# Performance work log

Measured on AMD Instinct MI355X. Metric: run time of the kernel, lower is better.

Reference implementation:

```python
import jax, jax.numpy as jnp
import numpy as np
from jax import lax

DS = 4  # downsample_factor

def setup_inputs() -> dict:
    key = jax.random.key(0)
    ks = jax.random.split(key, 7)
    B, C, H, W = 4, 256, 256, 256
    Cq = C // 16  # reduction=16
    return {
        "x":  jax.random.normal(ks[0], (B, C, H, W), dtype=jnp.float32),
        "Wq": jax.random.normal(ks[1], (Cq, C), dtype=jnp.float32) * 0.05,
        "bq": jax.random.normal(ks[2], (Cq,), dtype=jnp.float32) * 0.05,
        "Wk": jax.random.normal(ks[3], (Cq, C), dtype=jnp.float32) * 0.05,
        "bk": jax.random.normal(ks[4], (Cq,), dtype=jnp.float32) * 0.05,
        "Wv": jax.random.normal(ks[5], (C, C), dtype=jnp.float32) * 0.05,
        "bv": jax.random.normal(ks[6], (C,), dtype=jnp.float32) * 0.05,
    }

def reference(x, Wq, bq, Wk, bk, Wv, bv):
    B, C, H, W = x.shape
    # MaxPool2d(kernel=DS, stride=DS)
    xd = lax.reduce_window(x, -jnp.inf, lax.max,
                           (1, 1, DS, DS), (1, 1, DS, DS), 'VALID')
    h, w = xd.shape[2], xd.shape[3]
    N = h * w
    # 1x1 convs == channel-wise linear maps
    q = jnp.einsum('oc,bchw->bohw', Wq, xd) + bq[None, :, None, None]
    k = jnp.einsum('oc,bchw->bohw', Wk, xd) + bk[None, :, None, None]
    v = jnp.einsum('oc,bchw->bohw', Wv, xd) + bv[None, :, None, None]
    query = q.reshape(B, -1, N).transpose(0, 2, 1)   # [B, N, Cq]
    key_  = k.reshape(B, -1, N)                      # [B, Cq, N]
    value = v.reshape(B, C, N).transpose(0, 2, 1)    # [B, N, C]
    att = jnp.einsum('bnc,bcm->bnm', query, key_)    # [B, N, N]
    # global-mean threshold masking (zeros, not -inf, per original)
    att = jnp.where(att < att.mean(), 0.0, att)
    att = jax.nn.softmax(att, axis=-1)
    out = jnp.einsum('bnm,bmc->bnc', att, value)     # [B, N, C]
    out = out.transpose(0, 2, 1).reshape(B, C, h, w)
    # bilinear upsample, align_corners=False (half-pixel centers)
    out = jax.image.resize(out, (B, C, H, W), method='bilinear')
    return out + x
```

## Files before the change

### kernel.cpp

```cpp
#include <hip/hip_runtime.h>
#include <hip/hip_bf16.h>
#include <cmath>
#include <cstdint>
#include <cstddef>

typedef unsigned short u16;
typedef __attribute__((ext_vector_type(8))) __bf16 bf16x8;
typedef __attribute__((ext_vector_type(4))) float f32x4;
typedef __attribute__((ext_vector_type(8))) unsigned short us8;
typedef __attribute__((ext_vector_type(4))) unsigned short us4;

static const size_t OFF_XD32  = 0;
static const size_t OFF_QT    = 16777216;
static const size_t OFF_KHI   = 17825792;
static const size_t OFF_KLO   = 18350080;
static const size_t OFF_VT    = 18874368;
static const size_t OFF_WF    = 27262976;
static const size_t OFF_SPART = 27394048;

__device__ __forceinline__ void gl2lds16(const void* gsrc, void* ldst) {
  __builtin_amdgcn_global_load_lds(
      (const __attribute__((address_space(1))) unsigned int*)gsrc,
      (__attribute__((address_space(3))) unsigned int*)ldst, 16, 0, 0);
}

__device__ __forceinline__ float hmax4(float4 v) {
  return fmaxf(fmaxf(v.x, v.y), fmaxf(v.z, v.w));
}

__device__ __forceinline__ float bf2f(u16 u) {
  return __bfloat162float(__builtin_bit_cast(__hip_bfloat16, u));
}

__global__ __launch_bounds__(256) void k_pre(const float* __restrict__ x,
                                             const float* __restrict__ Wv,
                                             float* __restrict__ xd32,
                                             u16* __restrict__ Wf) {
  const int tid = threadIdx.x;
  if (blockIdx.x < 16) {
    const int rt = blockIdx.x;
#pragma unroll
    for (int i = 0; i < 2; ++i) {
      int s = tid + i * 256;
      int ks = s >> 6, lane = s & 63;
      const float* src = Wv + (size_t)(rt * 16 + (lane & 15)) * 256u + ks * 32 + (lane >> 4) * 8;
      float4 a = *reinterpret_cast<const float4*>(src);
      float4 b = *reinterpret_cast<const float4*>(src + 4);
      us8 o;
      o[0] = __builtin_bit_cast(u16, __float2bfloat16(a.x));
      o[1] = __builtin_bit_cast(u16, __float2bfloat16(a.y));
      o[2] = __builtin_bit_cast(u16, __float2bfloat16(a.z));
      o[3] = __builtin_bit_cast(u16, __float2bfloat16(a.w));
      o[4] = __builtin_bit_cast(u16, __float2bfloat16(b.x));
      o[5] = __builtin_bit_cast(u16, __float2bfloat16(b.y));
      o[6] = __builtin_bit_cast(u16, __float2bfloat16(b.z));
      o[7] = __builtin_bit_cast(u16, __float2bfloat16(b.w));
      *reinterpret_cast<us8*>(Wf + ((size_t)((rt * 8 + ks) * 64 + lane)) * 8u) = o;
    }
  } else {
    unsigned idx = (blockIdx.x - 16) * 256u + tid;
    unsigned xo = idx & 63u;
    unsigned yo = (idx >> 6) & 63u;
    unsigned bc = idx >> 12;
    const float* base = x + (size_t)bc * 65536u + yo * 1024u + xo * 4u;
    float m = -1e30f;
#pragma unroll
    for (int dy = 0; dy < 4; ++dy) {
      float4 v = *reinterpret_cast<const float4*>(base + dy * 256);
      m = fmaxf(m, hmax4(v));
    }
    xd32[(size_t)bc * 4096u + yo * 64u + xo] = m;
  }
}

__global__ __launch_bounds__(512) void k_qkv(const float* __restrict__ xd32,
                                             const u16* __restrict__ Wf, const float* __restrict__ bv,
                                             const float* __restrict__ Wq, const float* __restrict__ bq,
                                             const float* __restrict__ Wk, const float* __restrict__ bk,
                                             float* __restrict__ qT,
                                             u16* __restrict__ khi, u16* __restrict__ klo,
                                             u16* __restrict__ vT, float* __restrict__ Spart) {
  __shared__ char smem[65536];
  const int tid = threadIdx.x;

  if (blockIdx.x < 256) {
    u16 (*Bf)[8][64][8] = reinterpret_cast<u16(*)[8][64][8]>(smem);
    const int blk = blockIdx.x;
    const int b = blk >> 6, n0 = (blk & 63) * 64;
    const int w = tid >> 6, lane = tid & 63;

#pragma unroll
    for (int p = 0; p < 8; ++p) {
      int idx = p * 512 + tid;
      int k = idx >> 4, q4 = idx & 15;
      float4 v = *reinterpret_cast<const float4*>(
          xd32 + ((size_t)b * 256 + k) * 4096u + n0 + q4 * 4);
      int ks = k >> 5, kl = (k >> 3) & 3, j = k & 7;
      int ct = q4 >> 2, nb = (q4 & 3) * 4;
      Bf[ct][ks][kl * 16 + nb + 0][j] = __builtin_bit_cast(u16, __float2bfloat16(v.x));
      Bf[ct][ks][kl * 16 + nb + 1][j] = __builtin_bit_cast(u16, __float2bfloat16(v.y));
      Bf[ct][ks][kl * 16 + nb + 2][j] = __builtin_bit_cast(u16, __float2bfloat16(v.z));
      Bf[ct][ks][kl * 16 + nb + 3][j] = __builtin_bit_cast(u16, __float2bfloat16(v.w));
    }
    __syncthreads();

    f32x4 acc[2][4];
#pragma unroll
    for (int r = 0; r < 2; ++r)
#pragma unroll
      for (int ct = 0; ct < 4; ++ct) acc[r][ct] = (f32x4){0.f, 0.f, 0.f, 0.f};
    for (int ks = 0; ks < 8; ++ks) {
      bf16x8 Bv[4];
#pragma unroll
      for (int ct = 0; ct < 4; ++ct)
        Bv[ct] = __builtin_bit_cast(bf16x8, *reinterpret_cast<const us8*>(&Bf[ct][ks][lane][0]));
#pragma unroll
      for (int r = 0; r < 2; ++r) {
        int rt = w * 2 + r;
        bf16x8 Av = __builtin_bit_cast(bf16x8,
            *reinterpret_cast<const us8*>(Wf + ((size_t)((rt * 8 + ks) * 64 + lane)) * 8u));
#pragma unroll
        for (int ct = 0; ct < 4; ++ct)
          acc[r][ct] = __builtin_amdgcn_mfma_f32_16x16x32_bf16(Av, Bv[ct], acc[r][ct], 0, 0, 0);
      }
    }

#pragma unroll
    for (int r = 0; r < 2; ++r) {
      int row0 = (w * 2 + r) * 16 + (lane >> 4) * 4;
#pragma unroll
      for (int rr = 0; rr < 4; ++rr) {
        int c = row0 + rr;
        float bb = bv[c];
        u16* dst = vT + ((size_t)b * 256 + c) * 4096u + n0 + (lane & 15);
#pragma unroll
        for (int ct = 0; ct < 4; ++ct)
          dst[ct * 16] = __builtin_bit_cast(u16, __float2bfloat16(acc[r][ct][rr] + bb));
      }
    }
  } else {
    float (*xs)[64] = reinterpret_cast<float(*)[64]>(smem);
    const int qb = blockIdx.x - 256;
    const int b = qb >> 6, n0 = (qb & 63) * 64;
    {
      const float* src = xd32 + (size_t)b * 1048576u + n0;
#pragma unroll
      for (int i = 0; i < 8; ++i) {
        int slot = tid + i * 512;
        int c = slot >> 4, q4 = slot & 15;
        *reinterpret_cast<float4*>(&xs[c][q4 * 4]) =
            *reinterpret_cast<const float4*>(src + (size_t)c * 4096u + q4 * 4);
      }
    }
    __syncthreads();
    const int o = tid >> 4, t4 = tid & 15;
    const float* wrow = (o < 16) ? (Wq + (size_t)o * 256u) : (Wk + (size_t)(o - 16) * 256u);
    float a0 = 0.f, a1 = 0.f, a2 = 0.f, a3 = 0.f;
    for (int c = 0; c < 256; ++c) {
      float w = wrow[c];
      float4 xv = *reinterpret_cast<const float4*>(&xs[c][t4 * 4]);
      a0 = fmaf(w, xv.x, a0);
      a1 = fmaf(w, xv.y, a1);
      a2 = fmaf(w, xv.z, a2);
      a3 = fmaf(w, xv.w, a3);
    }
    int oo = (o < 16) ? o : (o - 16);
    float bb = (o < 16) ? bq[oo] : bk[oo];
    float v0 = a0 + bb, v1 = a1 + bb, v2 = a2 + bb, v3 = a3 + bb;
    size_t base = ((size_t)b * 4096u + n0 + t4 * 4) * 16u + oo;
    if (o < 16) {
      qT[base]      = v0;
      qT[base + 16] = v1;
      qT[base + 32] = v2;
      qT[base + 48] = v3;
    } else {
      float vv[4] = {v0, v1, v2, v3};
#pragma unroll
      for (int j = 0; j < 4; ++j) {
        __hip_bfloat16 h = __float2bfloat16(vv[j]);
        float fh = __bfloat162float(h);
        __hip_bfloat16 lo = __float2bfloat16(vv[j] - fh);
        khi[base + 16 * j] = __builtin_bit_cast(u16, h);
        klo[base + 16 * j] = __builtin_bit_cast(u16, lo);
      }
    }
    float s = a0 + a1 + a2 + a3;
    s += __shfl_xor(s, 1); s += __shfl_xor(s, 2);
    s += __shfl_xor(s, 4); s += __shfl_xor(s, 8);
    if (t4 == 0) Spart[(size_t)qb * 32u + o] = s;
  }
}

__global__ __launch_bounds__(512, 4) void k_flash(const float* __restrict__ qT,
                                                  const u16* __restrict__ khi,
                                                  const u16* __restrict__ klo,
                                                  const u16* __restrict__ vT,
                                                  const float* __restrict__ Spart,
                                                  const float* __restrict__ bq,
                                                  const float* __restrict__ bk,
                                                  u16* __restrict__ odsb) {
  __shared__ u16 vbuf[16384];
  __shared__ u16 kfh[4][64][8];
  __shared__ u16 kfl[4][64][8];
  __shared__ u16 pfr[4][2][64][8];
  __shared__ float scs[4];
  __shared__ float Ls[4][4][4];
  __shared__ float mean_s;

  const int orig = blockIdx.x;
  const int b    = (orig >> 1) & 3;
  const int row0 = (((orig & 1) << 5) | (orig >> 3)) * 64;
  const int tid  = threadIdx.x;
  const int w    = tid >> 6;
  const int lane = tid & 63;
  const int wq   = w & 3;
  const int wc   = w >> 2;
  const int g    = lane >> 4;
  const int c16  = lane & 15;
  const bool is_cw = (w < 4);

  if (tid >= 256 && tid < 320) {
    int t64 = tid - 256;
    int bb = t64 >> 4, o = t64 & 15;
    float sq = 4096.0f * bq[o], sk = 4096.0f * bk[o];
    for (int s = 0; s < 64; ++s) {
      const float* p = Spart + ((size_t)(bb * 64 + s)) * 32u;
      sq += p[o];
      sk += p[16 + o];
    }
    float pr = sq * sk;
#pragma unroll
    for (int off = 32; off > 0; off >>= 1) pr += __shfl_down(pr, off);
    if (t64 == 0) mean_s = pr * (1.0f / 67108864.0f);
  }

  float qv[16];
  {
    const float* qrow = qT + ((size_t)b*4096 + row0 + 16*wq + c16) * 16;
#pragma unroll
    for (int i = 0; i < 4; ++i) {
      float4 t4 = reinterpret_cast<const float4*>(qrow)[i];
      qv[4*i] = t4.x; qv[4*i+1] = t4.y; qv[4*i+2] = t4.z; qv[4*i+3] = t4.w;
    }
  }
  u16 qhi[16], qlo[16];
#pragma unroll
  for (int i = 0; i < 16; ++i) {
    __hip_bfloat16 h = __float2bfloat16(qv[i]);
    float fh = __bfloat162float(h);
    __hip_bfloat16 lo = __float2bfloat16(qv[i] - fh);
    qhi[i] = __builtin_bit_cast(u16, h);
    qlo[i] = __builtin_bit_cast(u16, lo);
  }
  us8 a1u, a2u;
  {
    const bool koff8  = (g & 1);
    const bool lo_src = (g >= 2);
#pragma unroll
    for (int i = 0; i < 8; ++i) {
      u16 hs = koff8 ? qhi[i+8] : qhi[i];
      u16 ls = koff8 ? qlo[i+8] : qlo[i];
      a1u[i] = lo_src ? ls : hs;
      a2u[i] = lo_src ? (u16)0 : hs;
    }
  }
  const bf16x8 A1 = __builtin_bit_cast(bf16x8, a1u);
  const bf16x8 A2 = __builtin_bit_cast(bf16x8, a2u);

  f32x4 O[8];
#pragma unroll
  for (int i = 0; i < 8; ++i) O[i] = (f32x4){0.f, 0.f, 0.f, 0.f};
  float Lr[4] = {0.f, 0.f, 0.f, 0.f};
  float M = 0.0f;

  const int tid2 = tid - 256;
  const int kv_s = tid2 >> 2, t4v = tid2 & 3;
  const int ks = kv_s >> 4, kld0 = (kv_s & 15) + 16*(t4v >> 1), ki0 = 4*(t4v & 1);

  {
    const u16* vsrc = vT + (size_t)b*256*4096;
#pragma unroll
    for (int i = 0; i < 4; ++i) {
      int u = i*512 + tid;
      int row = u >> 3, slot = u & 7;
      int sb = (slot*16) ^ ((row & 7) << 4);
      gl2lds16((const char*)(vsrc + (size_t)row*4096) + sb, (char*)&vbuf[0] + u*16);
    }
    if (tid >= 256) {
      size_t kb = ((size_t)b*4096 + kv_s)*16 + 4*t4v;
      us4 h4 = *reinterpret_cast<const us4*>(khi + kb);
      us4 l4 = *reinterpret_cast<const us4*>(klo + kb);
      *reinterpret_cast<us4*>(&kfh[ks][kld0][ki0])    = h4;
      *reinterpret_cast<us4*>(&kfh[ks][kld0+32][ki0]) = h4;
      *reinterpret_cast<us4*>(&kfl[ks][kld0][ki0])    = l4;
      *reinterpret_cast<us4*>(&kfl[ks][kld0+32][ki0]) = l4;
    }
  }
  __syncthreads();
  const float mean = mean_s;

  for (int t = 0; t < 64; ++t) {
    const int kv0n = ((t + 1) & 63) * 64;

    us4 hvec, lvec;
    if (tid >= 256) {
      size_t kb = ((size_t)b*4096 + kv0n + kv_s)*16 + 4*t4v;
      hvec = *reinterpret_cast<const us4*>(khi + kb);
      lvec = *reinterpret_cast<const us4*>(klo + kb);
    }

    if (is_cw) {
      f32x4 S[4];
#pragma unroll
      for (int s = 0; s < 4; ++s) {
        bf16x8 bh = __builtin_bit_cast(bf16x8, *reinterpret_cast<const us8*>(&kfh[s][lane][0]));
        bf16x8 bl = __builtin_bit_cast(bf16x8, *reinterpret_cast<const us8*>(&kfl[s][lane][0]));
        f32x4 acc = (f32x4){0.f, 0.f, 0.f, 0.f};
        acc = __builtin_amdgcn_mfma_f32_16x16x32_bf16(A1, bh, acc, 0, 0, 0);
        acc = __builtin_amdgcn_mfma_f32_16x16x32_bf16(A2, bl, acc, 0, 0, 0);
        S[s] = acc;
      }

      float pmax = -1e30f;
#pragma unroll
      for (int s = 0; s < 4; ++s)
#pragma unroll
        for (int r = 0; r < 4; ++r) {
          float v = S[s][r];
          v = (v < mean) ? 0.f : v;
          S[s][r] = v;
          pmax = fmaxf(pmax, v);
        }
      float sc_out = 1.0f;
      if (!__all(pmax <= M + 8.0f)) {
        float mw = pmax;
#pragma unroll
        for (int off = 1; off < 64; off <<= 1) mw = fmaxf(mw, __shfl_xor(mw, off));
        float Mn = fmaxf(M, mw);
        float sc = __expf(M - Mn);
#pragma unroll
        for (int i = 0; i < 8; ++i) {
          O[i][0] *= sc; O[i][1] *= sc; O[i][2] *= sc; O[i][3] *= sc;
        }
#pragma unroll
        for (int r = 0; r < 4; ++r) Lr[r] *= sc;
        M = Mn;
        sc_out = sc;
      }
      if (lane == 0) scs[wq] = sc_out;

      u16 pb[4][4];
#pragma unroll
      for (int s = 0; s < 4; ++s)
#pragma unroll
        for (int r = 0; r < 4; ++r) {
          float p = __expf(S[s][r] - M);
          Lr[r] += p;
          pb[s][r] = __builtin_bit_cast(u16, __float2bfloat16(p));
        }

      {
        const int ib = lane & 7;
        const int t1 = (lane >> 3) & 1;
#pragma unroll
        for (int s = 0; s < 4; ++s) {
          const int c2 = s >> 1;
          const int ldb = 16 * ((2*s + t1) & 3) + 4*g;
#pragma unroll
          for (int r = 0; r < 4; ++r) pfr[wq][c2][ldb + r][ib] = pb[s][r];
        }
      }
    }
    __syncthreads();

    if (!is_cw) {
      float sc = scs[wq];
      if (sc != 1.0f) {
#pragma unroll
        for (int i = 0; i < 8; ++i) {
          O[i][0] *= sc; O[i][1] *= sc; O[i][2] *= sc; O[i][3] *= sc;
        }
      }
    }

#pragma unroll
    for (int c2 = 0; c2 < 2; ++c2) {
      bf16x8 pa = __builtin_bit_cast(bf16x8, *reinterpret_cast<const us8*>(&pfr[wq][c2][lane][0]));
#pragma unroll
      for (int ct = 0; ct < 8; ++ct) {
        int row = (wc*8 + ct)*16 + c16;
        int off = (c2*64 + g*16) ^ ((lane & 7) << 4);
        bf16x8 vb = __builtin_bit_cast(bf16x8,
            *reinterpret_cast<const us8*>((const char*)&vbuf[0] + row*128 + off));
        O[ct] = __builtin_amdgcn_mfma_f32_16x16x32_bf16(pa, vb, O[ct], 0, 0, 0);
      }
    }

    if (tid >= 256) {
      *reinterpret_cast<us4*>(&kfh[ks][kld0][ki0])    = hvec;
      *reinterpret_cast<us4*>(&kfh[ks][kld0+32][ki0]) = hvec;
      *reinterpret_cast<us4*>(&kfl[ks][kld0][ki0])    = lvec;
      *reinterpret_cast<us4*>(&kfl[ks][kld0+32][ki0]) = lvec;
    }

    __syncthreads();

    if (t < 63) {
      const u16* vsrc = vT + (size_t)b*256*4096 + kv0n;
#pragma unroll
      for (int i = 0; i < 4; ++i) {
        int u = i*512 + tid;
        int row = u >> 3, slot = u & 7;
        int sb = (slot*16) ^ ((row & 7) << 4);
        gl2lds16((const char*)(vsrc + (size_t)row*4096) + sb, (char*)&vbuf[0] + u*16);
      }
    }
  }

  if (is_cw) {
#pragma unroll
    for (int r = 0; r < 4; ++r) {
      float v = Lr[r];
#pragma unroll
      for (int off = 1; off < 16; off <<= 1) v += __shfl_xor(v, off);
      Lr[r] = v;
    }
    if (c16 == 0) {
#pragma unroll
      for (int r = 0; r < 4; ++r) Ls[wq][g][r] = Lr[r];
    }
  }
  __syncthreads();
  float inv[4];
  if (is_cw) {
#pragma unroll
    for (int r = 0; r < 4; ++r) inv[r] = 1.0f / Lr[r];
  } else {
#pragma unroll
    for (int r = 0; r < 4; ++r) inv[r] = 1.0f / Ls[wq][g][r];
  }
#pragma unroll
  for (int ct = 0; ct < 8; ++ct) {
    int c = (wc*8 + ct)*16 + c16;
    u16* dst = odsb + ((size_t)b*256 + c) * 4096u + row0 + 16*wq + 4*g;
    us4 o4;
#pragma unroll
    for (int r = 0; r < 4; ++r)
      o4[r] = __builtin_bit_cast(u16, __float2bfloat16(O[ct][r] * inv[r]));
    *reinterpret_cast<us4*>(dst) = o4;
  }
}

__global__ __launch_bounds__(256) void k_up(const u16* __restrict__ ods, const float* __restrict__ x,
                                            float* __restrict__ out) {
  unsigned idx4 = blockIdx.x * 256u + threadIdx.x;
  int a  = (int)(idx4 & 63u);
  int i  = (int)((idx4 >> 6) & 255u);
  size_t bc = idx4 >> 14;

  float py = (i + 0.5f) * 0.25f - 0.5f;
  float y0f = floorf(py);
  float wy = py - y0f;
  int y0 = (int)y0f, y1 = y0 + 1;
  y0 = max(y0, 0); y1 = min(y1, 63);

  int xm1 = max(a - 1, 0), xp1 = min(a + 1, 63);

  const u16* r0 = ods + bc * 4096u + y0 * 64;
  const u16* r1 = ods + bc * 4096u + y1 * 64;
  float wy1 = 1.f - wy;
  float vm1 = wy1 * bf2f(r0[xm1]) + wy * bf2f(r1[xm1]);
  float v0  = wy1 * bf2f(r0[a])   + wy * bf2f(r1[a]);
  float vp1 = wy1 * bf2f(r0[xp1]) + wy * bf2f(r1[xp1]);

  float4 xv = *reinterpret_cast<const float4*>(x + (size_t)idx4 * 4u);
  float4 o4;
  o4.x = fmaf(0.375f, vm1, 0.625f * v0) + xv.x;
  o4.y = fmaf(0.125f, vm1, 0.875f * v0) + xv.y;
  o4.z = fmaf(0.875f, v0, 0.125f * vp1) + xv.z;
  o4.w = fmaf(0.625f, v0, 0.375f * vp1) + xv.w;
  *reinterpret_cast<float4*>(out + (size_t)idx4 * 4u) = o4;
}

extern "C" void kernel_launch(void* const* d_in, const int* in_sizes, int n_in,
                              void* d_out, int out_size, void* d_ws, size_t ws_size,
                              hipStream_t stream) {
  const float* x  = (const float*)d_in[0];
  const float* Wq = (const float*)d_in[1];
  const float* bq = (const float*)d_in[2];
  const float* Wk = (const float*)d_in[3];
  const float* bk = (const float*)d_in[4];
  const float* Wv = (const float*)d_in[5];
  const float* bv = (const float*)d_in[6];
  float* out = (float*)d_out;

  char* ws = (char*)d_ws;
  float* xd32  = (float*)(ws + OFF_XD32);
  float* qT    = (float*)(ws + OFF_QT);
  u16*   khi   = (u16*)(ws + OFF_KHI);
  u16*   klo   = (u16*)(ws + OFF_KLO);
  u16*   vT    = (u16*)(ws + OFF_VT);
  u16*   Wf    = (u16*)(ws + OFF_WF);
  float* Spart = (float*)(ws + OFF_SPART);
  u16*   odsb  = (u16*)(ws + OFF_XD32);

  k_pre<<<dim3(16400), dim3(256), 0, stream>>>(x, Wv, xd32, Wf);
  k_qkv<<<dim3(512), dim3(512), 0, stream>>>(xd32, Wf, bv, Wq, bq, Wk, bk, qT, khi, klo, vT, Spart);
  k_flash<<<dim3(256), dim3(512), 0, stream>>>(qT, khi, klo, vT, Spart, bq, bk, odsb);
  k_up<<<dim3(65536), dim3(256), 0, stream>>>(odsb, x, out);
}
```

Measured before the change: 243.8 us.

## Split flash attention into 512 smaller blocks of 32 query rows

Reorganizes the flash-attention kernel so each block has 256 threads (4 waves) and handles 32 query rows instead of 64, doubling the grid to 512 blocks. The goal is to fill more CUs on the device, since 256 blocks underfill the machine. Each block now streams the full V and K tiles for only half as many rows, which doubles total K/V traffic from L2. Thread-to-work mappings for the K and V loads are adjusted accordingly.

```diff
diff --git a/kernel.cpp b/kernel.cpp
--- a/kernel.cpp
+++ b/kernel.cpp
@@ -191,7 +191,7 @@
   }
 }
 
-__global__ __launch_bounds__(512, 4) void k_flash(const float* __restrict__ qT,
+__global__ __launch_bounds__(256, 3) void k_flash(const float* __restrict__ qT,
                                                   const u16* __restrict__ khi,
                                                   const u16* __restrict__ klo,
                                                   const u16* __restrict__ vT,
@@ -202,25 +202,26 @@
   __shared__ u16 vbuf[16384];
   __shared__ u16 kfh[4][64][8];
   __shared__ u16 kfl[4][64][8];
-  __shared__ u16 pfr[4][2][64][8];
-  __shared__ float scs[4];
-  __shared__ float Ls[4][4][4];
+  __shared__ u16 pfr[2][2][64][8];
+  __shared__ float scs[2];
+  __shared__ float Ls[2][4][4];
   __shared__ float mean_s;
 
   const int orig = blockIdx.x;
   const int b    = (orig >> 1) & 3;
-  const int row0 = (((orig & 1) << 5) | (orig >> 3)) * 64;
+  const int rowt = ((orig & 1) << 6) | (orig >> 3);
+  const int row0 = rowt * 32;
   const int tid  = threadIdx.x;
   const int w    = tid >> 6;
   const int lane = tid & 63;
-  const int wq   = w & 3;
-  const int wc   = w >> 2;
+  const int wq   = w & 1;
+  const int wc   = w >> 1;
   const int g    = lane >> 4;
   const int c16  = lane & 15;
-  const bool is_cw = (w < 4);
-
-  if (tid >= 256 && tid < 320) {
-    int t64 = tid - 256;
+  const bool is_cw = (w < 2);
+
+  if (tid >= 128 && tid < 192) {
+    int t64 = tid - 128;
     int bb = t64 >> 4, o = t64 & 15;
     float sq = 4096.0f * bq[o], sk = 4096.0f * bk[o];
     for (int s = 0; s < 64; ++s) {
@@ -273,27 +274,39 @@
   float Lr[4] = {0.f, 0.f, 0.f, 0.f};
   float M = 0.0f;
 
-  const int tid2 = tid - 256;
-  const int kv_s = tid2 >> 2, t4v = tid2 & 3;
-  const int ks = kv_s >> 4, kld0 = (kv_s & 15) + 16*(t4v >> 1), ki0 = 4*(t4v & 1);
+  const int tid2 = tid - 128;
+  int ksA[2], kldA[2], kiA[2], kvA[2];
+#pragma unroll
+  for (int h = 0; h < 2; ++h) {
+    int s = tid2 + h * 128;
+    int kv_s = s >> 2, t4v = s & 3;
+    kvA[h] = kv_s;
+    ksA[h] = kv_s >> 4;
+    kldA[h] = (kv_s & 15) + 16 * (t4v >> 1);
+    kiA[h] = 4 * (t4v & 1);
+  }
 
   {
     const u16* vsrc = vT + (size_t)b*256*4096;
 #pragma unroll
-    for (int i = 0; i < 4; ++i) {
-      int u = i*512 + tid;
+    for (int i = 0; i < 8; ++i) {
+      int u = i*256 + tid;
       int row = u >> 3, slot = u & 7;
       int sb = (slot*16) ^ ((row & 7) << 4);
       gl2lds16((const char*)(vsrc + (size_t)row*4096) + sb, (char*)&vbuf[0] + u*16);
     }
-    if (tid >= 256) {
-      size_t kb = ((size_t)b*4096 + kv_s)*16 + 4*t4v;
-      us4 h4 = *reinterpret_cast<const us4*>(khi + kb);
-      us4 l4 = *reinterpret_cast<const us4*>(klo + kb);
-      *reinterpret_cast<us4*>(&kfh[ks][kld0][ki0])    = h4;
-      *reinterpret_cast<us4*>(&kfh[ks][kld0+32][ki0]) = h4;
-      *reinterpret_cast<us4*>(&kfl[ks][kld0][ki0])    = l4;
-      *reinterpret_cast<us4*>(&kfl[ks][kld0+32][ki0]) = l4;
+    if (tid >= 128) {
+#pragma unroll
+      for (int h = 0; h < 2; ++h) {
+        int s = tid2 + h * 128;
+        size_t kb = ((size_t)b*4096 + kvA[h])*16 + 4*(s & 3);
+        us4 h4 = *reinterpret_cast<const us4*>(khi + kb);
+        us4 l4 = *reinterpret_cast<const us4*>(klo + kb);
+        *reinterpret_cast<us4*>(&kfh[ksA[h]][kldA[h]][kiA[h]])      = h4;
+        *reinterpret_cast<us4*>(&kfh[ksA[h]][kldA[h]+32][kiA[h]])   = h4;
+        *reinterpret_cast<us4*>(&kfl[ksA[h]][kldA[h]][kiA[h]])      = l4;
+        *reinterpret_cast<us4*>(&kfl[ksA[h]][kldA[h]+32][kiA[h]])   = l4;
+      }
     }
   }
   __syncthreads();
@@ -302,11 +315,15 @@
   for (int t = 0; t < 64; ++t) {
     const int kv0n = ((t + 1) & 63) * 64;
 
-    us4 hvec, lvec;
-    if (tid >= 256) {
-      size_t kb = ((size_t)b*4096 + kv0n + kv_s)*16 + 4*t4v;
-      hvec = *reinterpret_cast<const us4*>(khi + kb);
-      lvec = *reinterpret_cast<const us4*>(klo + kb);
+    us4 hvec[2], lvec[2];
+    if (tid >= 128) {
+#pragma unroll
+      for (int h = 0; h < 2; ++h) {
+        int s = tid2 + h * 128;
+        size_t kb = ((size_t)b*4096 + kv0n + kvA[h])*16 + 4*(s & 3);
+        hvec[h] = *reinterpret_cast<const us4*>(khi + kb);
+        lvec[h] = *reinterpret_cast<const us4*>(klo + kb);
+      }
     }
 
     if (is_cw) {
@@ -396,11 +413,14 @@
       }
     }
 
-    if (tid >= 256) {
-      *reinterpret_cast<us4*>(&kfh[ks][kld0][ki0])    = hvec;
-      *reinterpret_cast<us4*>(&kfh[ks][kld0+32][ki0]) = hvec;
-      *reinterpret_cast<us4*>(&kfl[ks][kld0][ki0])    = lvec;
-      *reinterpret_cast<us4*>(&kfl[ks][kld0+32][ki0]) = lvec;
+    if (tid >= 128) {
+#pragma unroll
+      for (int h = 0; h < 2; ++h) {
+        *reinterpret_cast<us4*>(&kfh[ksA[h]][kldA[h]][kiA[h]])      = hvec[h];
+        *reinterpret_cast<us4*>(&kfh[ksA[h]][kldA[h]+32][kiA[h]])   = hvec[h];
+        *reinterpret_cast<us4*>(&kfl[ksA[h]][kldA[h]][kiA[h]])      = lvec[h];
+        *reinterpret_cast<us4*>(&kfl[ksA[h]][kldA[h]+32][kiA[h]])   = lvec[h];
+      }
     }
 
     __syncthreads();
@@ -408,8 +428,8 @@
     if (t < 63) {
       const u16* vsrc = vT + (size_t)b*256*4096 + kv0n;
 #pragma unroll
-      for (int i = 0; i < 4; ++i) {
-        int u = i*512 + tid;
+      for (int i = 0; i < 8; ++i) {
+        int u = i*256 + tid;
         int row = u >> 3, slot = u & 7;
         int sb = (slot*16) ^ ((row & 7) << 4);
         gl2lds16((const char*)(vsrc + (size_t)row*4096) + sb, (char*)&vbuf[0] + u*16);
@@ -506,6 +526,6 @@
 
   k_pre<<<dim3(16400), dim3(256), 0, stream>>>(x, Wv, xd32, Wf);
   k_qkv<<<dim3(512), dim3(512), 0, stream>>>(xd32, Wf, bv, Wq, bq, Wk, bk, qT, khi, klo, vT, Spart);
-  k_flash<<<dim3(256), dim3(512), 0, stream>>>(qT, khi, klo, vT, Spart, bq, bk, odsb);
+  k_flash<<<dim3(512), dim3(256), 0, stream>>>(qT, khi, klo, vT, Spart, bq, bk, odsb);
   k_up<<<dim3(65536), dim3(256), 0, stream>>>(odsb, x, out);
 }
```

After: 275.0 us. 1.13x slower.
